# Performance work log

Measured on AMD Instinct MI355X. Metric: run time of the kernel, lower is better.

Reference implementation:

```python
import jax, jax.numpy as jnp
import numpy as np

MARGIN = 0.3
EPS = 1e-6  # torch pairwise_distance eps (added to the difference before norm)


def _sample_triplets(labels, B):
    """Vectorized equivalent of the per-row nonzero()+randint() mining loop.

    pos_idx[i] ~ Uniform{j : labels[j] == labels[i]}   (always non-empty: i itself)
    neg_idx[i] ~ Uniform{j : labels[j] != labels[i]}, fallback Uniform[0,B) if empty.
    Uniform-noise argmax over the masked set == uniform random choice.
    """
    key = jax.random.key(42)
    k1, k2, k3 = jax.random.split(key, 3)
    eq = labels[:, None] == labels[None, :]              # [B, B]
    pos_idx = jnp.argmax(jnp.where(eq, jax.random.uniform(k1, (B, B)), -1.0), axis=1)
    neg_scores = jnp.where(~eq, jax.random.uniform(k2, (B, B)), -1.0)
    has_neg = jnp.any(~eq, axis=1)
    neg_idx = jnp.where(has_neg,
                        jnp.argmax(neg_scores, axis=1),
                        jax.random.randint(k3, (B,), 0, B))
    return pos_idx, neg_idx


def _pdist(X, A, D):
    """out[i, j] = || A[j] - X[i] + EPS ||_2  (torch pairwise_distance semantics),
    computed via gram matrices instead of a [B,B,D] intermediate:
    ||a - x + eps||^2 = ||a||^2 + ||x||^2 - 2 a.x + 2*eps*(sum a - sum x) + D*eps^2.
    """
    sq = (jnp.sum(A * A, axis=1)[None, :]
          + jnp.sum(X * X, axis=1)[:, None]
          - 2.0 * (X @ A.T)
          + 2.0 * EPS * (jnp.sum(A, axis=1)[None, :] - jnp.sum(X, axis=1)[:, None])
          + D * EPS * EPS)
    return jnp.sqrt(jnp.maximum(sq, 1e-12))


def setup_inputs() -> dict:
    key = jax.random.key(0)
    kf, kl = jax.random.split(key)
    B, D, NUM_IDS = 4096, 1024, 512
    features = jax.random.normal(kf, (B, D), dtype=jnp.float32)
    labels = jax.random.randint(kl, (B,), 0, NUM_IDS, dtype=jnp.int32)
    return {"features": features, "labels": labels}


def reference(features, labels):
    B, D = features.shape
    pos_idx, neg_idx = _sample_triplets(labels, B)
    P = features[pos_idx]   # positives, [B, D]
    N = features[neg_idx]   # negatives, [B, D]
    # Original torch code stacks positives/negatives as [B,1,D] vs anchors [B,D],
    # so TripletMarginLoss broadcasts to ALL-PAIRS [B,B] distances:
    # dap[i, j] = ||anchor_j - positive_i + eps||, same for dan.
    dap = _pdist(P, features, D)  # [B, B]
    dan = _pdist(N, features, D)  # [B, B]
    return jnp.mean(jax.nn.relu(dap - dan + MARGIN))
```

## Files before the change

### kernel.cpp

```cpp
#include <hip/hip_runtime.h>
#include <stdint.h>

#define BSZ 4096
#define DIM 1024
#define EPSV 1e-6f
#define MARGINV 0.3f
#define SROWS 4
#define GEMM_BLOCKS 528
#define SAMPLE_BLOCKS (BSZ / SROWS)

#define TF_ROT(x0, x1, r) { x0 += x1; x1 = ((x1 << r) | (x1 >> (32 - r))); x1 ^= x0; }

__host__ __device__ __forceinline__ void threefry2x32(uint32_t k0, uint32_t k1,
                                                      uint32_t c0, uint32_t c1,
                                                      uint32_t& o0, uint32_t& o1) {
  uint32_t ks2 = k0 ^ k1 ^ 0x1BD11BDAu;
  uint32_t x0 = c0 + k0;
  uint32_t x1 = c1 + k1;
  TF_ROT(x0, x1, 13) TF_ROT(x0, x1, 15) TF_ROT(x0, x1, 26) TF_ROT(x0, x1, 6)
  x0 += k1;  x1 += ks2 + 1u;
  TF_ROT(x0, x1, 17) TF_ROT(x0, x1, 29) TF_ROT(x0, x1, 16) TF_ROT(x0, x1, 24)
  x0 += ks2; x1 += k0 + 2u;
  TF_ROT(x0, x1, 13) TF_ROT(x0, x1, 15) TF_ROT(x0, x1, 26) TF_ROT(x0, x1, 6)
  x0 += k0;  x1 += k1 + 3u;
  TF_ROT(x0, x1, 17) TF_ROT(x0, x1, 29) TF_ROT(x0, x1, 16) TF_ROT(x0, x1, 24)
  x0 += k1;  x1 += ks2 + 4u;
  TF_ROT(x0, x1, 13) TF_ROT(x0, x1, 15) TF_ROT(x0, x1, 26) TF_ROT(x0, x1, 6)
  x0 += ks2; x1 += k0 + 5u;
  o0 = x0; o1 = x1;
}

#define TFR2(r) { xa0 += xa1; xb0 += xb1; \
                  xa1 = ((xa1 << r) | (xa1 >> (32 - r))) ^ xa0; \
                  xb1 = ((xb1 << r) | (xb1 >> (32 - r))) ^ xb0; }

__device__ __forceinline__ void threefry_x2(uint32_t k0, uint32_t k1,
                                            uint32_t ca, uint32_t cb,
                                            uint32_t& oa, uint32_t& ob) {
  const uint32_t ks2 = k0 ^ k1 ^ 0x1BD11BDAu;
  uint32_t xa0 = k0, xa1 = ca + k1;
  uint32_t xb0 = k0, xb1 = cb + k1;
  TFR2(13) TFR2(15) TFR2(26) TFR2(6)
  xa0 += k1;  xa1 += ks2 + 1u;  xb0 += k1;  xb1 += ks2 + 1u;
  TFR2(17) TFR2(29) TFR2(16) TFR2(24)
  xa0 += ks2; xa1 += k0 + 2u;   xb0 += ks2; xb1 += k0 + 2u;
  TFR2(13) TFR2(15) TFR2(26) TFR2(6)
  xa0 += k0;  xa1 += k1 + 3u;   xb0 += k0;  xb1 += k1 + 3u;
  TFR2(17) TFR2(29) TFR2(16) TFR2(24)
  xa0 += k1;  xa1 += ks2 + 4u;  xb0 += k1;  xb1 += ks2 + 4u;
  TFR2(13) TFR2(15) TFR2(26) TFR2(6)
  xa0 += ks2; xa1 += k0 + 5u;   xb0 += ks2; xb1 += k0 + 5u;
  oa = xa0 ^ xa1;
  ob = xb0 ^ xb1;
}

__device__ __forceinline__ uint16_t f2bf(float f) {
  uint32_t u = __float_as_uint(f);
  u += 0x7FFFu + ((u >> 16) & 1u);
  return (uint16_t)(u >> 16);
}

__global__ __launch_bounds__(256) void prep_kernel(const float* __restrict__ F,
                                                   uint8_t* __restrict__ Fq,
                                                   float* __restrict__ norm2,
                                                   float* __restrict__ sums,
                                                   float* __restrict__ nv) {
  const int w = threadIdx.x >> 6, l = threadIdx.x & 63;
  const int r = blockIdx.x * 4 + w;
  const float4* src = (const float4*)(F + (size_t)r * DIM);
  uint32_t* dst = (uint32_t*)(Fq + (size_t)r * DIM);
  float s = 0.f, q = 0.f;
#pragma unroll
  for (int c = 0; c < 4; ++c) {
    float4 v = src[c * 64 + l];
    s += (v.x + v.y) + (v.z + v.w);
    q += v.x * v.x + v.y * v.y + v.z * v.z + v.w * v.w;
    int wd = 0;
    wd = __builtin_amdgcn_cvt_pk_fp8_f32(v.x, v.y, wd, false);
    wd = __builtin_amdgcn_cvt_pk_fp8_f32(v.z, v.w, wd, true);
    dst[c * 64 + l] = (uint32_t)wd;
  }
  for (int off = 32; off; off >>= 1) { s += __shfl_xor(s, off); q += __shfl_xor(q, off); }
  if (l == 0) {
    norm2[r] = q; sums[r] = s;
    nv[r] = q + 2.0f * EPSV * s;
  }
}

using int8v = __attribute__((ext_vector_type(8))) int;
using int4v = __attribute__((ext_vector_type(4))) int;
using f32x4 = __attribute__((ext_vector_type(4))) float;

__device__ __forceinline__ void async_load16(const void* g, void* l) {
  __builtin_amdgcn_global_load_lds((__attribute__((address_space(1))) void*)g,
                                   (__attribute__((address_space(3))) void*)l, 16, 0, 0);
}

__global__ __launch_bounds__(256, 4) void gemm_sample_kernel(
    const uint8_t* __restrict__ Fq, uint16_t* __restrict__ Gb,
    const int* __restrict__ labels, int* __restrict__ pos_idx, int* __restrict__ neg_idx,
    uint32_t p0, uint32_t p1, uint32_t n0, uint32_t n1) {
  __shared__ __align__(16) uint8_t lA[128 * 128];
  __shared__ __align__(16) uint8_t lB[128 * 128];
  const int t = threadIdx.x;

  if (blockIdx.x >= GEMM_BLOCKS) {
    int* plist = (int*)lA;
    int* pcnt = (int*)(lA + SROWS * 64 * 4);
    unsigned long long* swp = (unsigned long long*)(lB);
    unsigned long long* swn = (unsigned long long*)(lB + 64);
    const int i0 = (blockIdx.x - GEMM_BLOCKS) * SROWS;
    if (t < SROWS) { pcnt[t] = 0; swp[t] = 0ull; swn[t] = 0ull; }
    int lj[16];
#pragma unroll
    for (int c = 0; c < 16; ++c) lj[c] = labels[c * 256 + t];
    __syncthreads();
    const int lane = t & 63;
#pragma unroll 1
    for (int r = 0; r < SROWS; ++r) {
      const int li = labels[i0 + r];
      const uint32_t base = (uint32_t)(i0 + r) * (uint32_t)BSZ + (uint32_t)t;
      uint32_t bestn = 0u;
#pragma unroll
      for (int c = 0; c < 16; c += 2) {
        uint32_t bitsA, bitsB;
        threefry_x2(n0, n1, base + (uint32_t)(c * 256), base + (uint32_t)((c + 1) * 256),
                    bitsA, bitsB);
        const uint32_t packA = ((bitsA >> 5) & 0xFFFFFFF0u) | (uint32_t)(15 - c);
        const uint32_t packB = ((bitsB >> 5) & 0xFFFFFFF0u) | (uint32_t)(14 - c);
        const uint32_t vA = (lj[c] == li) ? 0u : packA;
        const uint32_t vB = (lj[c + 1] == li) ? 0u : packB;
        const uint32_t m = vA > vB ? vA : vB;
        if (m > bestn) bestn = m;
      }
      unsigned long long keyn = 0ull;
      if (bestn) {
        const int c = 15 - (int)(bestn & 15u);
        const int j = c * 256 + t;
        keyn = ((unsigned long long)(bestn >> 4) << 32) | (uint32_t)(~j);
      }
      for (int off = 32; off; off >>= 1) {
        unsigned long long o = __shfl_xor(keyn, off);
        if (o > keyn) keyn = o;
      }
      if (lane == 0) atomicMax(&swn[r], keyn);
#pragma unroll
      for (int c = 0; c < 16; ++c) {
        if (lj[c] == li) {
          int sl = atomicAdd(&pcnt[r], 1);
          if (sl < 64) plist[r * 64 + sl] = c * 256 + t;
        }
      }
    }
    __syncthreads();
    const int w = t >> 6;
    {
      const int cnt = pcnt[w] < 64 ? pcnt[w] : 64;
      if (lane < cnt) {
        const int j = plist[w * 64 + lane];
        uint32_t y0, y1;
        threefry2x32(p0, p1, 0u, (uint32_t)(i0 + w) * (uint32_t)BSZ + (uint32_t)j, y0, y1);
        const unsigned long long key =
            ((unsigned long long)((y0 ^ y1) >> 9) << 32) | (uint32_t)(~j);
        atomicMax(&swp[w], key);
      }
    }
    __syncthreads();
    if (t < SROWS) {
      pos_idx[i0 + t] = (int)(~(uint32_t)swp[t]);
      const unsigned long long vn = swn[t];
      neg_idx[i0 + t] = (vn == 0ull) ? 0 : (int)(~(uint32_t)vn);
    }
    return;
  }

  const int p = blockIdx.x;
  int by = (int)((sqrtf(8.0f * (float)p + 1.0f) - 1.0f) * 0.5f);
  if ((by + 1) * (by + 2) / 2 <= p) ++by;
  if (by * (by + 1) / 2 > p) --by;
  const int bx = p - by * (by + 1) / 2;

  const int l = t & 63;
  const int w = t >> 6;
  const int wm = (w >> 1) * 64;
  const int wn = (w & 1) * 64;
  const int bm = bx * 128;
  const int bn = by * 128;

  f32x4 acc[4][4] = {};

  const int srow = t >> 3;
  const int scol = (((t & 7) ^ ((t >> 3) & 7)) << 4);
  const uint8_t* gA0 = Fq + (size_t)(bm + srow) * DIM + scol;
  const uint8_t* gB0 = Fq + (size_t)(bn + srow) * DIM + scol;

  const int fr = l & 15;
  const int c0 = (l >> 4) * 2;
  int offA[4][2], offB[4][2];
#pragma unroll
  for (int tm = 0; tm < 4; ++tm) {
    const int fra = wm + tm * 16 + fr, sw = fra & 7;
    offA[tm][0] = fra * 128 + ((c0 ^ sw) << 4);
    offA[tm][1] = fra * 128 + (((c0 + 1) ^ sw) << 4);
    const int frb = wn + tm * 16 + fr, sb = frb & 7;
    offB[tm][0] = frb * 128 + ((c0 ^ sb) << 4);
    offB[tm][1] = frb * 128 + (((c0 + 1) ^ sb) << 4);
  }

  for (int it = 0; it < 8; ++it) {
    const int k0 = it * 128;
    __syncthreads();
#pragma unroll
    for (int ld = 0; ld < 4; ++ld) {
      async_load16(gA0 + (size_t)ld * 32 * DIM + k0, (char*)lA + (ld * 256 + t) * 16);
      async_load16(gB0 + (size_t)ld * 32 * DIM + k0, (char*)lB + (ld * 256 + t) * 16);
    }
    __syncthreads();
    int8v av[4], bv[4];
#pragma unroll
    for (int tm = 0; tm < 4; ++tm) {
      int4v alo = *(const int4v*)&lA[offA[tm][0]];
      int4v ahi = *(const int4v*)&lA[offA[tm][1]];
      av[tm] = __builtin_shufflevector(alo, ahi, 0, 1, 2, 3, 4, 5, 6, 7);
      int4v blo = *(const int4v*)&lB[offB[tm][0]];
      int4v bhi = *(const int4v*)&lB[offB[tm][1]];
      bv[tm] = __builtin_shufflevector(blo, bhi, 0, 1, 2, 3, 4, 5, 6, 7);
    }
#pragma unroll
    for (int tm = 0; tm < 4; ++tm)
#pragma unroll
      for (int tn = 0; tn < 4; ++tn)
        acc[tm][tn] = __builtin_amdgcn_mfma_scale_f32_16x16x128_f8f6f4(
            av[tm], bv[tn], acc[tm][tn],
            0, 0,
            0, 0x7F7F7F7F,
            0, 0x7F7F7F7F);
  }
  const int cr = (l >> 4) * 4;
  const int cc = l & 15;
#pragma unroll
  for (int tm = 0; tm < 4; ++tm)
#pragma unroll
    for (int tn = 0; tn < 4; ++tn) {
      const int row0 = bm + wm + tm * 16 + cr;
      const int col  = bn + wn + tn * 16 + cc;
      ushort h0 = f2bf(acc[tm][tn][0]), h1 = f2bf(acc[tm][tn][1]);
      ushort h2 = f2bf(acc[tm][tn][2]), h3 = f2bf(acc[tm][tn][3]);
      Gb[(size_t)(row0 + 0) * BSZ + col] = h0;
      Gb[(size_t)(row0 + 1) * BSZ + col] = h1;
      Gb[(size_t)(row0 + 2) * BSZ + col] = h2;
      Gb[(size_t)(row0 + 3) * BSZ + col] = h3;
      ushort4 v = make_ushort4(h0, h1, h2, h3);
      *(ushort4*)&Gb[(size_t)col * BSZ + row0] = v;
    }
}

__device__ __forceinline__ float bfl(uint32_t w) { return __uint_as_float(w << 16); }
__device__ __forceinline__ float bfh(uint32_t w) { return __uint_as_float(w & 0xFFFF0000u); }

__global__ __launch_bounds__(256) void loss_kernel(const uint16_t* __restrict__ Gb,
                                                   const float* __restrict__ norm2,
                                                   const float* __restrict__ sums,
                                                   const float* __restrict__ nv,
                                                   const int* __restrict__ pos_idx,
                                                   const int* __restrict__ neg_idx,
                                                   float* __restrict__ partial) {
  const int i = blockIdx.x, t = threadIdx.x;
  const int a = pos_idx[i], b = neg_idx[i];
  const float deps2 = (float)DIM * EPSV * EPSV;
  const float ca = norm2[a] - 2.0f * EPSV * sums[a] + deps2;
  const float cb = norm2[b] - 2.0f * EPSV * sums[b] + deps2;
  const uint4* Ga = (const uint4*)(Gb + (size_t)a * BSZ);
  const uint4* Gn = (const uint4*)(Gb + (size_t)b * BSZ);
  const float4* N4 = (const float4*)nv;
  uint4 ga[2], gn[2];
  float4 njv[4];
  ga[0] = Ga[t * 2]; ga[1] = Ga[t * 2 + 1];
  gn[0] = Gn[t * 2]; gn[1] = Gn[t * 2 + 1];
#pragma unroll
  for (int k = 0; k < 4; ++k) njv[k] = N4[t * 4 + k];
  float s = 0.f;
#pragma unroll
  for (int h = 0; h < 2; ++h) {
    const uint4 gau = ga[h], gnu = gn[h];
    float gav[8] = {bfl(gau.x), bfh(gau.x), bfl(gau.y), bfh(gau.y),
                    bfl(gau.z), bfh(gau.z), bfl(gau.w), bfh(gau.w)};
    float gnv[8] = {bfl(gnu.x), bfh(gnu.x), bfl(gnu.y), bfh(gnu.y),
                    bfl(gnu.z), bfh(gnu.z), bfl(gnu.w), bfh(gnu.w)};
    const float4 na = njv[h * 2], nb = njv[h * 2 + 1];
    float nj[8] = {na.x, na.y, na.z, na.w, nb.x, nb.y, nb.z, nb.w};
#pragma unroll
    for (int e = 0; e < 8; ++e) {
      const float dap = sqrtf(fmaxf(fmaf(-2.f, gav[e], nj[e] + ca), 1e-12f));
      const float dan = sqrtf(fmaxf(fmaf(-2.f, gnv[e], nj[e] + cb), 1e-12f));
      s += fmaxf(dap - dan + MARGINV, 0.f);
    }
  }
  for (int off = 32; off; off >>= 1) s += __shfl_xor(s, off);
  __shared__ float ps[4];
  const int w = t >> 6, lane = t & 63;
  if (lane == 0) ps[w] = s;
  __syncthreads();
  if (t == 0) partial[i] = (ps[0] + ps[1]) + (ps[2] + ps[3]);
}

__global__ __launch_bounds__(256) void finalize_kernel(const float* __restrict__ partial,
                                                       float* __restrict__ out) {
  const int t = threadIdx.x;
  const float4* P4 = (const float4*)partial;
  float s = 0.f;
#pragma unroll
  for (int k = 0; k < 4; ++k) {
    float4 v = P4[k * 256 + t];
    s += (v.x + v.y) + (v.z + v.w);
  }
  for (int off = 32; off; off >>= 1) s += __shfl_xor(s, off);
  __shared__ float ps[4];
  const int w = t >> 6, lane = t & 63;
  if (lane == 0) ps[w] = s;
  __syncthreads();
  if (t == 0)
    out[0] = ((ps[0] + ps[1]) + (ps[2] + ps[3])) * (1.0f / ((float)BSZ * (float)BSZ));
}

extern "C" void kernel_launch(void* const* d_in, const int* in_sizes, int n_in,
                              void* d_out, int out_size, void* d_ws, size_t ws_size,
                              hipStream_t stream) {
  const float* feat = (const float*)d_in[0];
  const int* labels = (const int*)d_in[1];
  float* out = (float*)d_out;

  char* ws = (char*)d_ws;
  uint16_t* Gb     = (uint16_t*)ws;
  uint8_t* Fq      = (uint8_t*)(ws + (size_t)33554432);
  float* norm2     = (float*)(ws + (size_t)37748736);
  float* sums      = (float*)(ws + (size_t)37748736 + 16384);
  float* nv        = (float*)(ws + (size_t)37748736 + 32768);
  int* pos_idx     = (int*)  (ws + (size_t)37748736 + 49152);
  int* neg_idx     = (int*)  (ws + (size_t)37748736 + 65536);
  float* partial   = (float*)(ws + (size_t)37748736 + 81920);

  uint32_t k1a, k1b, k2a, k2b;
  threefry2x32(0u, 42u, 0u, 0u, k1a, k1b);
  threefry2x32(0u, 42u, 0u, 1u, k2a, k2b);

  prep_kernel<<<dim3(BSZ / 4), dim3(256), 0, stream>>>(feat, Fq, norm2, sums, nv);
  gemm_sample_kernel<<<dim3(GEMM_BLOCKS + SAMPLE_BLOCKS), dim3(256), 0, stream>>>(
      Fq, Gb, labels, pos_idx, neg_idx, k1a, k1b, k2a, k2b);
  loss_kernel<<<dim3(BSZ), dim3(256), 0, stream>>>(Gb, norm2, sums, nv, pos_idx,
                                                   neg_idx, partial);
  finalize_kernel<<<dim3(1), dim3(256), 0, stream>>>(partial, out);
}
```

Before: 136.1 us.

## Move triplet sampling into prep kernel and process several rows per loss block

The triplet-sampling blocks move out of the GEMM launch and into the feature-prep launch. The GEMM kernel then runs only its 528 tiles, with no sampling tail competing for CUs or inflating its shared-memory footprint. The sampling work now overlaps the memory-bound fp8 conversion instead. The loss kernel also handles 4 anchor rows per block, reusing the nv vector loads across rows at the cost of fewer blocks and extra barriers.

```diff
diff --git a/kernel.cpp b/kernel.cpp
--- a/kernel.cpp
+++ b/kernel.cpp
@@ -6,8 +6,11 @@
 #define EPSV 1e-6f
 #define MARGINV 0.3f
 #define SROWS 4
+#define LROWS 4
 #define GEMM_BLOCKS 528
 #define SAMPLE_BLOCKS (BSZ / SROWS)
+#define PREP_BLOCKS (BSZ / 4)
+#define LOSS_BLOCKS (BSZ / LROWS)
 
 #define TF_ROT(x0, x1, r) { x0 += x1; x1 = ((x1 << r) | (x1 >> (32 - r))); x1 ^= x0; }
 
@@ -60,30 +63,102 @@
   return (uint16_t)(u >> 16);
 }
 
-__global__ __launch_bounds__(256) void prep_kernel(const float* __restrict__ F,
-                                                   uint8_t* __restrict__ Fq,
-                                                   float* __restrict__ norm2,
-                                                   float* __restrict__ sums,
-                                                   float* __restrict__ nv) {
-  const int w = threadIdx.x >> 6, l = threadIdx.x & 63;
-  const int r = blockIdx.x * 4 + w;
-  const float4* src = (const float4*)(F + (size_t)r * DIM);
-  uint32_t* dst = (uint32_t*)(Fq + (size_t)r * DIM);
-  float s = 0.f, q = 0.f;
-#pragma unroll
-  for (int c = 0; c < 4; ++c) {
-    float4 v = src[c * 64 + l];
-    s += (v.x + v.y) + (v.z + v.w);
-    q += v.x * v.x + v.y * v.y + v.z * v.z + v.w * v.w;
-    int wd = 0;
-    wd = __builtin_amdgcn_cvt_pk_fp8_f32(v.x, v.y, wd, false);
-    wd = __builtin_amdgcn_cvt_pk_fp8_f32(v.z, v.w, wd, true);
-    dst[c * 64 + l] = (uint32_t)wd;
-  }
-  for (int off = 32; off; off >>= 1) { s += __shfl_xor(s, off); q += __shfl_xor(q, off); }
-  if (l == 0) {
-    norm2[r] = q; sums[r] = s;
-    nv[r] = q + 2.0f * EPSV * s;
+__global__ __launch_bounds__(256, 8) void prep_sample_kernel(
+    const float* __restrict__ F, uint8_t* __restrict__ Fq,
+    float* __restrict__ norm2, float* __restrict__ sums, float* __restrict__ nv,
+    const int* __restrict__ labels, int* __restrict__ pos_idx, int* __restrict__ neg_idx,
+    uint32_t p0, uint32_t p1, uint32_t n0, uint32_t n1) {
+  __shared__ int plist[SROWS * 64];
+  __shared__ int pcnt[SROWS];
+  __shared__ unsigned long long swp[SROWS];
+  __shared__ unsigned long long swn[SROWS];
+  const int t = threadIdx.x;
+
+  if (blockIdx.x >= SAMPLE_BLOCKS) {
+    const int w = t >> 6, l = t & 63;
+    const int r = (blockIdx.x - SAMPLE_BLOCKS) * 4 + w;
+    const float4* src = (const float4*)(F + (size_t)r * DIM);
+    uint32_t* dst = (uint32_t*)(Fq + (size_t)r * DIM);
+    float s = 0.f, q = 0.f;
+#pragma unroll
+    for (int c = 0; c < 4; ++c) {
+      float4 v = src[c * 64 + l];
+      s += (v.x + v.y) + (v.z + v.w);
+      q += v.x * v.x + v.y * v.y + v.z * v.z + v.w * v.w;
+      int wd = 0;
+      wd = __builtin_amdgcn_cvt_pk_fp8_f32(v.x, v.y, wd, false);
+      wd = __builtin_amdgcn_cvt_pk_fp8_f32(v.z, v.w, wd, true);
+      dst[c * 64 + l] = (uint32_t)wd;
+    }
+    for (int off = 32; off; off >>= 1) { s += __shfl_xor(s, off); q += __shfl_xor(q, off); }
+    if (l == 0) {
+      norm2[r] = q; sums[r] = s;
+      nv[r] = q + 2.0f * EPSV * s;
+    }
+    return;
+  }
+
+  const int i0 = blockIdx.x * SROWS;
+  if (t < SROWS) { pcnt[t] = 0; swp[t] = 0ull; swn[t] = 0ull; }
+  int lj[16];
+#pragma unroll
+  for (int c = 0; c < 16; ++c) lj[c] = labels[c * 256 + t];
+  __syncthreads();
+  const int lane = t & 63;
+#pragma unroll 1
+  for (int r = 0; r < SROWS; ++r) {
+    const int li = labels[i0 + r];
+    const uint32_t base = (uint32_t)(i0 + r) * (uint32_t)BSZ + (uint32_t)t;
+    uint32_t bestn = 0u;
+#pragma unroll
+    for (int c = 0; c < 16; c += 2) {
+      uint32_t bitsA, bitsB;
+      threefry_x2(n0, n1, base + (uint32_t)(c * 256), base + (uint32_t)((c + 1) * 256),
+                  bitsA, bitsB);
+      const uint32_t packA = ((bitsA >> 5) & 0xFFFFFFF0u) | (uint32_t)(15 - c);
+      const uint32_t packB = ((bitsB >> 5) & 0xFFFFFFF0u) | (uint32_t)(14 - c);
+      const uint32_t vA = (lj[c] == li) ? 0u : packA;
+      const uint32_t vB = (lj[c + 1] == li) ? 0u : packB;
+      const uint32_t mab = vA > vB ? vA : vB;
+      bestn = bestn > mab ? bestn : mab;
+    }
+    unsigned long long keyn = 0ull;
+    if (bestn) {
+      const int c = 15 - (int)(bestn & 15u);
+      const int j = c * 256 + t;
+      keyn = ((unsigned long long)(bestn >> 4) << 32) | (uint32_t)(~j);
+    }
+    for (int off = 32; off; off >>= 1) {
+      unsigned long long o = __shfl_xor(keyn, off);
+      if (o > keyn) keyn = o;
+    }
+    if (lane == 0) atomicMax(&swn[r], keyn);
+#pragma unroll
+    for (int c = 0; c < 16; ++c) {
+      if (lj[c] == li) {
+        int sl = atomicAdd(&pcnt[r], 1);
+        if (sl < 64) plist[r * 64 + sl] = c * 256 + t;
+      }
+    }
+  }
+  __syncthreads();
+  const int w = t >> 6;
+  {
+    const int cnt = pcnt[w] < 64 ? pcnt[w] : 64;
+    if (lane < cnt) {
+      const int j = plist[w * 64 + lane];
+      uint32_t y0, y1;
+      threefry2x32(p0, p1, 0u, (uint32_t)(i0 + w) * (uint32_t)BSZ + (uint32_t)j, y0, y1);
+      const unsigned long long key =
+          ((unsigned long long)((y0 ^ y1) >> 9) << 32) | (uint32_t)(~j);
+      atomicMax(&swp[w], key);
+    }
+  }
+  __syncthreads();
+  if (t < SROWS) {
+    pos_idx[i0 + t] = (int)(~(uint32_t)swp[t]);
+    const unsigned long long vn = swn[t];
+    neg_idx[i0 + t] = (vn == 0ull) ? 0 : (int)(~(uint32_t)vn);
   }
 }
 
@@ -96,83 +171,11 @@
                                    (__attribute__((address_space(3))) void*)l, 16, 0, 0);
 }
 
-__global__ __launch_bounds__(256, 4) void gemm_sample_kernel(
-    const uint8_t* __restrict__ Fq, uint16_t* __restrict__ Gb,
-    const int* __restrict__ labels, int* __restrict__ pos_idx, int* __restrict__ neg_idx,
-    uint32_t p0, uint32_t p1, uint32_t n0, uint32_t n1) {
+__global__ __launch_bounds__(256, 4) void gemm_kernel(
+    const uint8_t* __restrict__ Fq, uint16_t* __restrict__ Gb) {
   __shared__ __align__(16) uint8_t lA[128 * 128];
   __shared__ __align__(16) uint8_t lB[128 * 128];
   const int t = threadIdx.x;
-
-  if (blockIdx.x >= GEMM_BLOCKS) {
-    int* plist = (int*)lA;
-    int* pcnt = (int*)(lA + SROWS * 64 * 4);
-    unsigned long long* swp = (unsigned long long*)(lB);
-    unsigned long long* swn = (unsigned long long*)(lB + 64);
-    const int i0 = (blockIdx.x - GEMM_BLOCKS) * SROWS;
-    if (t < SROWS) { pcnt[t] = 0; swp[t] = 0ull; swn[t] = 0ull; }
-    int lj[16];
-#pragma unroll
-    for (int c = 0; c < 16; ++c) lj[c] = labels[c * 256 + t];
-    __syncthreads();
-    const int lane = t & 63;
-#pragma unroll 1
-    for (int r = 0; r < SROWS; ++r) {
-      const int li = labels[i0 + r];
-      const uint32_t base = (uint32_t)(i0 + r) * (uint32_t)BSZ + (uint32_t)t;
-      uint32_t bestn = 0u;
-#pragma unroll
-      for (int c = 0; c < 16; c += 2) {
-        uint32_t bitsA, bitsB;
-        threefry_x2(n0, n1, base + (uint32_t)(c * 256), base + (uint32_t)((c + 1) * 256),
-                    bitsA, bitsB);
-        const uint32_t packA = ((bitsA >> 5) & 0xFFFFFFF0u) | (uint32_t)(15 - c);
-        const uint32_t packB = ((bitsB >> 5) & 0xFFFFFFF0u) | (uint32_t)(14 - c);
-        const uint32_t vA = (lj[c] == li) ? 0u : packA;
-        const uint32_t vB = (lj[c + 1] == li) ? 0u : packB;
-        const uint32_t m = vA > vB ? vA : vB;
-        if (m > bestn) bestn = m;
-      }
-      unsigned long long keyn = 0ull;
-      if (bestn) {
-        const int c = 15 - (int)(bestn & 15u);
-        const int j = c * 256 + t;
-        keyn = ((unsigned long long)(bestn >> 4) << 32) | (uint32_t)(~j);
-      }
-      for (int off = 32; off; off >>= 1) {
-        unsigned long long o = __shfl_xor(keyn, off);
-        if (o > keyn) keyn = o;
-      }
-      if (lane == 0) atomicMax(&swn[r], keyn);
-#pragma unroll
-      for (int c = 0; c < 16; ++c) {
-        if (lj[c] == li) {
-          int sl = atomicAdd(&pcnt[r], 1);
-          if (sl < 64) plist[r * 64 + sl] = c * 256 + t;
-        }
-      }
-    }
-    __syncthreads();
-    const int w = t >> 6;
-    {
-      const int cnt = pcnt[w] < 64 ? pcnt[w] : 64;
-      if (lane < cnt) {
-        const int j = plist[w * 64 + lane];
-        uint32_t y0, y1;
-        threefry2x32(p0, p1, 0u, (uint32_t)(i0 + w) * (uint32_t)BSZ + (uint32_t)j, y0, y1);
-        const unsigned long long key =
-            ((unsigned long long)((y0 ^ y1) >> 9) << 32) | (uint32_t)(~j);
-        atomicMax(&swp[w], key);
-      }
-    }
-    __syncthreads();
-    if (t < SROWS) {
-      pos_idx[i0 + t] = (int)(~(uint32_t)swp[t]);
-      const unsigned long long vn = swn[t];
-      neg_idx[i0 + t] = (vn == 0ull) ? 0 : (int)(~(uint32_t)vn);
-    }
-    return;
-  }
 
   const int p = blockIdx.x;
   int by = (int)((sqrtf(8.0f * (float)p + 1.0f) - 1.0f) * 0.5f);
@@ -265,43 +268,48 @@
                                                    const int* __restrict__ pos_idx,
                                                    const int* __restrict__ neg_idx,
                                                    float* __restrict__ partial) {
-  const int i = blockIdx.x, t = threadIdx.x;
-  const int a = pos_idx[i], b = neg_idx[i];
+  const int i0 = blockIdx.x * LROWS, t = threadIdx.x;
   const float deps2 = (float)DIM * EPSV * EPSV;
-  const float ca = norm2[a] - 2.0f * EPSV * sums[a] + deps2;
-  const float cb = norm2[b] - 2.0f * EPSV * sums[b] + deps2;
-  const uint4* Ga = (const uint4*)(Gb + (size_t)a * BSZ);
-  const uint4* Gn = (const uint4*)(Gb + (size_t)b * BSZ);
   const float4* N4 = (const float4*)nv;
-  uint4 ga[2], gn[2];
   float4 njv[4];
-  ga[0] = Ga[t * 2]; ga[1] = Ga[t * 2 + 1];
-  gn[0] = Gn[t * 2]; gn[1] = Gn[t * 2 + 1];
 #pragma unroll
   for (int k = 0; k < 4; ++k) njv[k] = N4[t * 4 + k];
-  float s = 0.f;
-#pragma unroll
-  for (int h = 0; h < 2; ++h) {
-    const uint4 gau = ga[h], gnu = gn[h];
-    float gav[8] = {bfl(gau.x), bfh(gau.x), bfl(gau.y), bfh(gau.y),
-                    bfl(gau.z), bfh(gau.z), bfl(gau.w), bfh(gau.w)};
-    float gnv[8] = {bfl(gnu.x), bfh(gnu.x), bfl(gnu.y), bfh(gnu.y),
-                    bfl(gnu.z), bfh(gnu.z), bfl(gnu.w), bfh(gnu.w)};
-    const float4 na = njv[h * 2], nb = njv[h * 2 + 1];
-    float nj[8] = {na.x, na.y, na.z, na.w, nb.x, nb.y, nb.z, nb.w};
-#pragma unroll
-    for (int e = 0; e < 8; ++e) {
-      const float dap = sqrtf(fmaxf(fmaf(-2.f, gav[e], nj[e] + ca), 1e-12f));
-      const float dan = sqrtf(fmaxf(fmaf(-2.f, gnv[e], nj[e] + cb), 1e-12f));
-      s += fmaxf(dap - dan + MARGINV, 0.f);
-    }
-  }
-  for (int off = 32; off; off >>= 1) s += __shfl_xor(s, off);
   __shared__ float ps[4];
   const int w = t >> 6, lane = t & 63;
-  if (lane == 0) ps[w] = s;
-  __syncthreads();
-  if (t == 0) partial[i] = (ps[0] + ps[1]) + (ps[2] + ps[3]);
+#pragma unroll 1
+  for (int r = 0; r < LROWS; ++r) {
+    const int i = i0 + r;
+    const int a = pos_idx[i], b = neg_idx[i];
+    const float ca = norm2[a] - 2.0f * EPSV * sums[a] + deps2;
+    const float cb = norm2[b] - 2.0f * EPSV * sums[b] + deps2;
+    const uint4* Ga = (const uint4*)(Gb + (size_t)a * BSZ);
+    const uint4* Gn = (const uint4*)(Gb + (size_t)b * BSZ);
+    uint4 ga[2], gn[2];
+    ga[0] = Ga[t * 2]; ga[1] = Ga[t * 2 + 1];
+    gn[0] = Gn[t * 2]; gn[1] = Gn[t * 2 + 1];
+    float s = 0.f;
+#pragma unroll
+    for (int h = 0; h < 2; ++h) {
+      const uint4 gau = ga[h], gnu = gn[h];
+      float gav[8] = {bfl(gau.x), bfh(gau.x), bfl(gau.y), bfh(gau.y),
+                      bfl(gau.z), bfh(gau.z), bfl(gau.w), bfh(gau.w)};
+      float gnv[8] = {bfl(gnu.x), bfh(gnu.x), bfl(gnu.y), bfh(gnu.y),
+                      bfl(gnu.z), bfh(gnu.z), bfl(gnu.w), bfh(gnu.w)};
+      const float4 na = njv[h * 2], nb = njv[h * 2 + 1];
+      float nj[8] = {na.x, na.y, na.z, na.w, nb.x, nb.y, nb.z, nb.w};
+#pragma unroll
+      for (int e = 0; e < 8; ++e) {
+        const float dap = sqrtf(fmaxf(fmaf(-2.f, gav[e], nj[e] + ca), 1e-12f));
+        const float dan = sqrtf(fmaxf(fmaf(-2.f, gnv[e], nj[e] + cb), 1e-12f));
+        s += fmaxf(dap - dan + MARGINV, 0.f);
+      }
+    }
+    for (int off = 32; off; off >>= 1) s += __shfl_xor(s, off);
+    if (lane == 0) ps[w] = s;
+    __syncthreads();
+    if (t == 0) partial[i] = (ps[0] + ps[1]) + (ps[2] + ps[3]);
+    __syncthreads();
+  }
 }
 
 __global__ __launch_bounds__(256) void finalize_kernel(const float* __restrict__ partial,
@@ -344,10 +352,10 @@
   threefry2x32(0u, 42u, 0u, 0u, k1a, k1b);
   threefry2x32(0u, 42u, 0u, 1u, k2a, k2b);
 
-  prep_kernel<<<dim3(BSZ / 4), dim3(256), 0, stream>>>(feat, Fq, norm2, sums, nv);
-  gemm_sample_kernel<<<dim3(GEMM_BLOCKS + SAMPLE_BLOCKS), dim3(256), 0, stream>>>(
-      Fq, Gb, labels, pos_idx, neg_idx, k1a, k1b, k2a, k2b);
-  loss_kernel<<<dim3(BSZ), dim3(256), 0, stream>>>(Gb, norm2, sums, nv, pos_idx,
-                                                   neg_idx, partial);
+  prep_sample_kernel<<<dim3(SAMPLE_BLOCKS + PREP_BLOCKS), dim3(256), 0, stream>>>(
+      feat, Fq, norm2, sums, nv, labels, pos_idx, neg_idx, k1a, k1b, k2a, k2b);
+  gemm_kernel<<<dim3(GEMM_BLOCKS), dim3(256), 0, stream>>>(Fq, Gb);
+  loss_kernel<<<dim3(LOSS_BLOCKS), dim3(256), 0, stream>>>(Gb, norm2, sums, nv,
+                                                           pos_idx, neg_idx, partial);
   finalize_kernel<<<dim3(1), dim3(256), 0, stream>>>(partial, out);
 }
```

Result: slower. 150.9 us (+10.9%).
